# Performance work log

Hardware: AMD Instinct MI355X
Metric: run time of the kernel (lower is better)

## Reference

```python
import jax, jax.numpy as jnp
import numpy as np

NUM_HEADS = 16
D_K = 64
BATCH_SIZE = 64
NUM_EDGES = 32768


def setup_inputs() -> dict:
    key = jax.random.key(0)
    k1, k2, k3, k4 = jax.random.split(key, 4)
    global_query = jax.random.normal(k1, (NUM_HEADS, BATCH_SIZE, D_K), dtype=jnp.float32)
    local_key = jax.random.normal(k2, (NUM_HEADS, NUM_EDGES, D_K), dtype=jnp.float32)
    local_value = jax.random.normal(k3, (NUM_HEADS, NUM_EDGES, D_K), dtype=jnp.float32)
    batch = jnp.sort(jax.random.randint(k4, (NUM_EDGES,), 0, BATCH_SIZE, dtype=jnp.int64))
    return {"global_query": global_query, "local_key": local_key,
            "local_value": local_value, "batch": batch}


def reference(global_query, local_key, local_value, batch):
    # global_query: [h, b, d]; local_key/value: [h, e, d]; batch: [e] segment ids
    num_heads, batch_size, d_k = global_query.shape
    # seg[b, e] = True iff edge e belongs to graph b
    seg = batch[None, :] == jnp.arange(batch_size, dtype=batch.dtype)[:, None]  # [b, e]
    # NOTE: original module does NOT scale by sqrt(d_k) despite its name
    scores = jnp.einsum('hbd,hed->hbe', global_query, local_key)  # [h, b, e]
    # per-segment softmax: out-of-segment entries get -inf -> exactly 0 weight,
    # matching the original which only softmaxes over edges with batch == i
    masked = jnp.where(seg[None, :, :], scores, -jnp.inf)
    attn = jax.nn.softmax(masked, axis=-1)  # [h, b, e]; zeros outside segment
    output = jnp.einsum('hbe,hed->hbd', attn, local_value)  # [h, b, d]
    return output, attn
```

## Files before the change

### kernel.cpp

```cpp
#include <hip/hip_runtime.h>
#include <math.h>

#define NH 16
#define NB 64
#define DK 64
#define NE 32768
#define BLOCK 512

typedef float vf4 __attribute__((ext_vector_type(4)));

__global__ void seg_bounds_kernel(const int* __restrict__ batch, int* __restrict__ bounds) {
    int e = blockIdx.x * 256 + threadIdx.x;
    if (e >= NE) return;
    int be = batch[e];
    if (e == 0) {
        for (int b = 0; b <= be; ++b) bounds[b] = 0;
    } else {
        int bp = batch[e - 1];
        for (int b = bp + 1; b <= be; ++b) bounds[b] = e;
    }
    if (e == NE - 1) {
        for (int b = be + 1; b <= NB; ++b) bounds[b] = NE;
    }
}

__global__ __launch_bounds__(BLOCK) void sdpa_seg_kernel(
    const float* __restrict__ Q,
    const float* __restrict__ K,
    const float* __restrict__ V,
    const int*   __restrict__ bounds,
    float* __restrict__ out,
    float* __restrict__ attn,
    float* __restrict__ ksc_base)
{
    const int b    = blockIdx.x;
    const int h    = blockIdx.y;
    const int tid  = threadIdx.x;
    const int wave = tid >> 6;
    const int lane = tid & 63;

    const int start = bounds[b];
    const int end   = bounds[b + 1];

    float* arow = attn + ((size_t)h * NB + b) * NE;
    float* ksc  = ksc_base + (size_t)h * NE;

    __shared__ float qs[DK];
    __shared__ float sm[8], sl[8];
    __shared__ float red[8][DK];

    if (tid < DK) qs[tid] = Q[((size_t)h * NB + b) * DK + tid];

    {
        vf4 z4 = (vf4)(0.f);
        vf4* arow4 = (vf4*)arow;
        for (int i = tid; i < NE / 4; i += BLOCK)
            __builtin_nontemporal_store(z4, arow4 + i);
    }
    __syncthreads();

    const float4* q4 = (const float4*)qs;
    float m = -INFINITY, l = 0.f;
    for (int e = start + tid; e < end; e += BLOCK) {
        const float4* kr = (const float4*)(K + ((size_t)h * NE + e) * DK);
        float sx = 0.f, sy = 0.f, sz = 0.f, sw = 0.f;
        #pragma unroll
        for (int i = 0; i < DK / 4; ++i) {
            float4 kv = kr[i];
            float4 qv = q4[i];
            sx = fmaf(kv.x, qv.x, sx);
            sy = fmaf(kv.y, qv.y, sy);
            sz = fmaf(kv.z, qv.z, sz);
            sw = fmaf(kv.w, qv.w, sw);
        }
        float s = (sx + sy) + (sz + sw);
        ksc[e] = s;
        float nm = fmaxf(m, s);
        l = l * __expf(m - nm) + __expf(s - nm);
        m = nm;
    }

    #pragma unroll
    for (int off = 32; off; off >>= 1) {
        float om = __shfl_xor(m, off);
        float ol = __shfl_xor(l, off);
        float nm = fmaxf(m, om);
        float t1 = (l  > 0.f) ? l  * __expf(m  - nm) : 0.f;
        float t2 = (ol > 0.f) ? ol * __expf(om - nm) : 0.f;
        m = nm; l = t1 + t2;
    }
    if (lane == 0) { sm[wave] = m; sl[wave] = l; }
    __syncthreads();

    float M = -INFINITY;
    #pragma unroll
    for (int w = 0; w < 8; ++w) M = fmaxf(M, sm[w]);
    float L = 0.f;
    #pragma unroll
    for (int w = 0; w < 8; ++w) L += (sl[w] > 0.f) ? sl[w] * __expf(sm[w] - M) : 0.f;
    const float inv = (L > 0.f) ? 1.f / L : 0.f;

    for (int e = start + tid; e < end; e += BLOCK)
        __builtin_nontemporal_store(__expf(ksc[e] - M) * inv, arow + e);

    const int S   = end - start;
    const int per = (S + 7) >> 3;
    const int cb  = start + wave * per;
    const int ce  = (cb + per < end) ? cb + per : end;

    float a0 = 0.f, a1 = 0.f, a2 = 0.f, a3 = 0.f;
    int e = cb;
    for (; e + 3 < ce; e += 4) {
        float p0 = __expf(ksc[e]     - M) * inv;
        float p1 = __expf(ksc[e + 1] - M) * inv;
        float p2 = __expf(ksc[e + 2] - M) * inv;
        float p3 = __expf(ksc[e + 3] - M) * inv;
        const float* vb = V + ((size_t)h * NE + e) * DK + lane;
        a0 = fmaf(p0, vb[0 * DK], a0);
        a1 = fmaf(p1, vb[1 * DK], a1);
        a2 = fmaf(p2, vb[2 * DK], a2);
        a3 = fmaf(p3, vb[3 * DK], a3);
    }
    for (; e < ce; ++e) {
        float p = __expf(ksc[e] - M) * inv;
        a0 = fmaf(p, V[((size_t)h * NE + e) * DK + lane], a0);
    }
    red[wave][lane] = (a0 + a1) + (a2 + a3);
    __syncthreads();
    if (wave == 0) {
        float r = 0.f;
        #pragma unroll
        for (int w = 0; w < 8; ++w) r += red[w][lane];
        out[((size_t)h * NB + b) * DK + lane] = r;
    }
}

extern "C" void kernel_launch(void* const* d_in, const int* in_sizes, int n_in,
                              void* d_out, int out_size, void* d_ws, size_t ws_size,
                              hipStream_t stream) {
    const float* Q     = (const float*)d_in[0];
    const float* K     = (const float*)d_in[1];
    const float* V     = (const float*)d_in[2];
    const int*   batch = (const int*)d_in[3];

    float* out  = (float*)d_out;
    float* attn = out + (size_t)NH * NB * DK;

    int*   bounds = (int*)d_ws;
    float* ksc    = (float*)d_ws + 128;

    seg_bounds_kernel<<<NE / 256, 256, 0, stream>>>(batch, bounds);

    dim3 grid(NB, NH);
    sdpa_seg_kernel<<<grid, BLOCK, 0, stream>>>(Q, K, V, bounds, out, attn, ksc);
}
```

Before: 339.2 us.

## Split fused attention kernel into scores, flat attn-write, and output kernels

Splits the single per-(batch,head) kernel into three launches. The first computes scores and the softmax stats (max, inverse sum) and stashes them in the output buffer. The second is a flat grid-wide kernel that writes the whole dense attn matrix, zeros included, with vectorized nontemporal stores. The third re-reads attn and V to form the output. This spreads the dominant 128MB zero-fill write across many small blocks instead of 1024 large blocks, at the cost of extra launches and re-reading attn values.

New measurement: 344.3 us. About the same (+1.5%).

```diff
diff --git a/kernel.cpp b/kernel.cpp
--- a/kernel.cpp
+++ b/kernel.cpp
@@ -5,9 +5,9 @@
 #define NB 64
 #define DK 64
 #define NE 32768
-#define BLOCK 512
 
 typedef float vf4 __attribute__((ext_vector_type(4)));
+
 
 __global__ void seg_bounds_kernel(const int* __restrict__ batch, int* __restrict__ bounds) {
     int e = blockIdx.x * 256 + threadIdx.x;
@@ -24,14 +24,12 @@
     }
 }
 
-__global__ __launch_bounds__(BLOCK) void sdpa_seg_kernel(
+__global__ __launch_bounds__(512) void scores_kernel(
     const float* __restrict__ Q,
     const float* __restrict__ K,
-    const float* __restrict__ V,
     const int*   __restrict__ bounds,
-    float* __restrict__ out,
-    float* __restrict__ attn,
-    float* __restrict__ ksc_base)
+    float* __restrict__ ksc_base,
+    float* __restrict__ stash)
 {
     const int b    = blockIdx.x;
     const int h    = blockIdx.y;
@@ -42,26 +40,17 @@
     const int start = bounds[b];
     const int end   = bounds[b + 1];
 
-    float* arow = attn + ((size_t)h * NB + b) * NE;
-    float* ksc  = ksc_base + (size_t)h * NE;
+    float* ksc = ksc_base + (size_t)h * NE;
 
     __shared__ float qs[DK];
     __shared__ float sm[8], sl[8];
-    __shared__ float red[8][DK];
 
     if (tid < DK) qs[tid] = Q[((size_t)h * NB + b) * DK + tid];
-
-    {
-        vf4 z4 = (vf4)(0.f);
-        vf4* arow4 = (vf4*)arow;
-        for (int i = tid; i < NE / 4; i += BLOCK)
-            __builtin_nontemporal_store(z4, arow4 + i);
-    }
     __syncthreads();
 
     const float4* q4 = (const float4*)qs;
     float m = -INFINITY, l = 0.f;
-    for (int e = start + tid; e < end; e += BLOCK) {
+    for (int e = start + tid; e < end; e += 512) {
         const float4* kr = (const float4*)(K + ((size_t)h * NE + e) * DK);
         float sx = 0.f, sy = 0.f, sz = 0.f, sw = 0.f;
         #pragma unroll
@@ -92,16 +81,64 @@
     if (lane == 0) { sm[wave] = m; sl[wave] = l; }
     __syncthreads();
 
-    float M = -INFINITY;
-    #pragma unroll
-    for (int w = 0; w < 8; ++w) M = fmaxf(M, sm[w]);
-    float L = 0.f;
-    #pragma unroll
-    for (int w = 0; w < 8; ++w) L += (sl[w] > 0.f) ? sl[w] * __expf(sm[w] - M) : 0.f;
-    const float inv = (L > 0.f) ? 1.f / L : 0.f;
+    if (tid == 0) {
+        float M = -INFINITY;
+        #pragma unroll
+        for (int w = 0; w < 8; ++w) M = fmaxf(M, sm[w]);
+        float L = 0.f;
+        #pragma unroll
+        for (int w = 0; w < 8; ++w) L += (sl[w] > 0.f) ? sl[w] * __expf(sm[w] - M) : 0.f;
+        const float inv = (L > 0.f) ? 1.f / L : 0.f;
+        stash[((size_t)h * NB + b) * DK + 0] = M;
+        stash[((size_t)h * NB + b) * DK + 1] = inv;
+    }
+}
 
-    for (int e = start + tid; e < end; e += BLOCK)
-        __builtin_nontemporal_store(__expf(ksc[e] - M) * inv, arow + e);
+__global__ __launch_bounds__(256) void attn_write_kernel(
+    const int*   __restrict__ batch,
+    const float* __restrict__ ksc_base,
+    const float* __restrict__ stash,
+    float* __restrict__ attn)
+{
+    const unsigned idx = blockIdx.x * 256u + threadIdx.x;
+    const int e4 = idx & (NE / 4 - 1);
+    const int bh = idx >> 13;
+    const int b  = bh & (NB - 1);
+    const int e0 = e4 << 2;
+
+    const int4 bt = *(const int4*)(batch + e0);
+    vf4 r = (vf4)(0.f);
+    if (bt.x == b || bt.y == b || bt.z == b || bt.w == b) {
+        const float M   = stash[(size_t)bh * DK + 0];
+        const float inv = stash[(size_t)bh * DK + 1];
+        const int h = bh >> 6;
+        const float4 s = *(const float4*)(ksc_base + (size_t)h * NE + e0);
+        if (bt.x == b) r.x = __expf(s.x - M) * inv;
+        if (bt.y == b) r.y = __expf(s.y - M) * inv;
+        if (bt.z == b) r.z = __expf(s.z - M) * inv;
+        if (bt.w == b) r.w = __expf(s.w - M) * inv;
+    }
+    __builtin_nontemporal_store(r, (vf4*)attn + idx);
+}
+
+__global__ __launch_bounds__(512) void out_kernel(
+    const float* __restrict__ V,
+    const int*   __restrict__ bounds,
+    const float* __restrict__ attn,
+    float* __restrict__ out)
+{
+    const int b    = blockIdx.x;
+    const int h    = blockIdx.y;
+    const int tid  = threadIdx.x;
+    const int wave = tid >> 6;
+    const int lane = tid & 63;
+
+    const int start = bounds[b];
+    const int end   = bounds[b + 1];
+
+    const float* arow = attn + ((size_t)h * NB + b) * NE;
+
+    __shared__ float red[8][DK];
 
     const int S   = end - start;
     const int per = (S + 7) >> 3;
@@ -111,10 +148,10 @@
     float a0 = 0.f, a1 = 0.f, a2 = 0.f, a3 = 0.f;
     int e = cb;
     for (; e + 3 < ce; e += 4) {
-        float p0 = __expf(ksc[e]     - M) * inv;
-        float p1 = __expf(ksc[e + 1] - M) * inv;
-        float p2 = __expf(ksc[e + 2] - M) * inv;
-        float p3 = __expf(ksc[e + 3] - M) * inv;
+        float p0 = arow[e];
+        float p1 = arow[e + 1];
+        float p2 = arow[e + 2];
+        float p3 = arow[e + 3];
         const float* vb = V + ((size_t)h * NE + e) * DK + lane;
         a0 = fmaf(p0, vb[0 * DK], a0);
         a1 = fmaf(p1, vb[1 * DK], a1);
@@ -122,7 +159,7 @@
         a3 = fmaf(p3, vb[3 * DK], a3);
     }
     for (; e < ce; ++e) {
-        float p = __expf(ksc[e] - M) * inv;
+        float p = arow[e];
         a0 = fmaf(p, V[((size_t)h * NE + e) * DK + lane], a0);
     }
     red[wave][lane] = (a0 + a1) + (a2 + a3);
@@ -152,5 +189,10 @@
     seg_bounds_kernel<<<NE / 256, 256, 0, stream>>>(batch, bounds);
 
     dim3 grid(NB, NH);
-    sdpa_seg_kernel<<<grid, BLOCK, 0, stream>>>(Q, K, V, bounds, out, attn, ksc);
+    scores_kernel<<<grid, 512, 0, stream>>>(Q, K, bounds, ksc, out);
+
+    const unsigned nvf4 = (unsigned)NH * NB * (NE / 4);
+    attn_write_kernel<<<nvf4 / 256, 256, 0, stream>>>(batch, ksc, out, attn);
+
+    out_kernel<<<grid, 512, 0, stream>>>(V, bounds, attn, out);
 }
```
